# Kernel optimization log

Hardware: AMD Instinct MI355X
Metric: run time of the kernel (lower is better)

## Reference

```python
import jax, jax.numpy as jnp
import numpy as np

N = 100000
E = 1600000
IN_FEATS = 256
OUT_FEATS = 128
THRESHOLD = 0.5


def setup_inputs() -> dict:
    key = jax.random.key(0)
    k1, k2, k3, k4, k5, k6, k7 = jax.random.split(key, 7)
    return {
        "feat": jax.random.normal(k1, (N, IN_FEATS), dtype=jnp.float32),
        "src": jax.random.randint(k2, (E,), 0, N, dtype=jnp.int32),
        "dst": jax.random.randint(k3, (E,), 0, N, dtype=jnp.int32),
        "edge_weight": jax.random.uniform(k4, (E,), dtype=jnp.float32),
        "weight": jax.random.normal(k5, (IN_FEATS, OUT_FEATS), dtype=jnp.float32),
        "bias": jax.random.normal(k6, (OUT_FEATS,), dtype=jnp.float32),
        "mask_real": jax.random.uniform(k7, (IN_FEATS, OUT_FEATS), dtype=jnp.float32),
    }


def reference(feat, src, dst, edge_weight, weight, bias, mask_real):
    ones_e = jnp.ones((E,), dtype=feat.dtype)
    # norm == 'both': scale source feats by out_degree^-0.5 (clamped at 1)
    out_deg = jnp.clip(jax.ops.segment_sum(ones_e, src, num_segments=N), 1.0)
    feat_src = feat * (out_deg ** -0.5)[:, None]  # [N, IN]
    # binarized mask with straight-through estimator (training-mode path)
    hard = (mask_real > THRESHOLD).astype(mask_real.dtype)
    mask_t = jax.lax.stop_gradient(hard - mask_real) + mask_real
    w = mask_t * weight  # [IN, OUT]
    # in_feats > out_feats: project before aggregation
    feat_src = feat_src @ w  # [N, OUT]
    # u_mul_e then sum: gather source feats, scale by edge weight, scatter-add to dst
    msgs = feat_src[src] * edge_weight[:, None]  # [E, OUT]
    rst = jax.ops.segment_sum(msgs, dst, num_segments=N)  # [N, OUT]
    # norm == 'both': scale by in_degree^-0.5 (clamped at 1)
    in_deg = jnp.clip(jax.ops.segment_sum(ones_e, dst, num_segments=N), 1.0)
    rst = rst * (in_deg ** -0.5)[:, None]
    return rst + bias
```

## Files before the change

### kernel.cpp

```cpp
#include <hip/hip_runtime.h>

#define N_NODES 100000
#define N_EDGES 1600000
#define IN_F 256
#define OUT_F 128
#define NBUCK 391
#define NPART 256
#define CHUNK (N_EDGES / NPART)
#define BCAP 5632

#define ODW 25000
#define ODRB ((ODW + 255) / 256)

typedef __attribute__((ext_vector_type(8))) short short8;
typedef __attribute__((ext_vector_type(4))) float f32x4;

__device__ __forceinline__ unsigned bf16_rne(float f) {
    unsigned u = __float_as_uint(f);
    return (u + 0x7fffu + ((u >> 16) & 1u)) >> 16;
}

__global__ __launch_bounds__(256) void fused_pre_kernel(const int* __restrict__ src,
                                                        const int* __restrict__ dst,
                                                        const float* __restrict__ weight,
                                                        const float* __restrict__ mask_real,
                                                        unsigned* __restrict__ part,
                                                        unsigned* __restrict__ hist,
                                                        unsigned short* __restrict__ wmT) {
    __shared__ unsigned h[ODW];
    __shared__ unsigned hh[NBUCK];
    int b = blockIdx.x, t = threadIdx.x;
    for (int i = t; i < ODW; i += 256) h[i] = 0u;
    for (int i = t; i < NBUCK; i += 256) hh[i] = 0u;
    if (t < 128) {
        int i = b * 128 + t;
        int k = i >> 7, n = i & 127;
        float v = (mask_real[i] > 0.5f) ? weight[i] : 0.0f;
        wmT[(size_t)n * IN_F + k] = (unsigned short)bf16_rne(v);
    }
    __syncthreads();
    int base = b * CHUNK;
    for (int i = t; i < CHUNK; i += 256) {
        unsigned s = (unsigned)src[base + i];
        unsigned d = (unsigned)dst[base + i];
        atomicAdd(&h[s >> 2], 1u << ((s & 3u) * 8u));
        atomicAdd(&hh[d >> 8], 1u);
    }
    __syncthreads();
    unsigned* op = part + (size_t)b * ODW;
    for (int i = t; i < ODW; i += 256) op[i] = h[i];
    for (int i = t; i < NBUCK; i += 256) hist[(size_t)b * NBUCK + i] = hh[i];
}

__global__ __launch_bounds__(256) void fused_reduce_kernel(const unsigned* __restrict__ part,
                                                           const unsigned* __restrict__ hist,
                                                           unsigned* __restrict__ outpk,
                                                           unsigned* __restrict__ bsum) {
    int t = threadIdx.x;
    if (blockIdx.x < ODRB) {
        int d = blockIdx.x * 256 + t;
        if (d < ODW) {
            unsigned sum = 0u;
#pragma unroll 8
            for (int b = 0; b < NPART; b++) sum += part[(size_t)b * ODW + d];
            outpk[d] = sum;
        }
    } else {
        __shared__ unsigned red[256];
        int b = blockIdx.x - ODRB;
        red[t] = hist[(size_t)t * NBUCK + b];
        __syncthreads();
#pragma unroll
        for (int d = 128; d > 0; d >>= 1) {
            if (t < d) red[t] += red[t + d];
            __syncthreads();
        }
        if (t == 0) bsum[b] = red[0];
    }
}

__global__ __launch_bounds__(256) void scan_apply_kernel(const unsigned* __restrict__ hist,
                                                         const unsigned* __restrict__ bsum,
                                                         unsigned* __restrict__ scanned) {
    __shared__ unsigned red[256];
    __shared__ unsigned part[256];
    int b = blockIdx.x, t = threadIdx.x;
    unsigned loc = 0u;
    for (int i = t; i < b; i += 256) loc += bsum[i];
    red[t] = loc;
    __syncthreads();
#pragma unroll
    for (int d = 128; d > 0; d >>= 1) {
        if (t < d) red[t] += red[t + d];
        __syncthreads();
    }
    unsigned bpref = red[0];
    unsigned v = hist[(size_t)t * NBUCK + b];
    part[t] = v;
    __syncthreads();
#pragma unroll
    for (int d = 1; d < 256; d <<= 1) {
        unsigned x = (t >= d) ? part[t - d] : 0u;
        __syncthreads();
        part[t] += x;
        __syncthreads();
    }
    scanned[(size_t)b * 256 + t] = bpref + part[t] - v;
}

__global__ __launch_bounds__(256) void scatter_kernel(const int* __restrict__ src,
                                                      const int* __restrict__ dst,
                                                      const float* __restrict__ ew,
                                                      const unsigned* __restrict__ scanned,
                                                      uint2* __restrict__ tmp) {
    __shared__ unsigned cur[NBUCK];
    int p = blockIdx.x, t = threadIdx.x;
    for (int b = t; b < NBUCK; b += 256) cur[b] = scanned[(size_t)b * 256 + p];
    __syncthreads();
    int base = p * CHUNK;
    for (int i = t; i < CHUNK; i += 256) {
        int e = base + i;
        int s = src[e];
        int d = dst[e];
        unsigned pos = atomicAdd(&cur[(unsigned)d >> 8], 1u);
        tmp[pos] = make_uint2((unsigned)s | (((unsigned)d & 255u) << 17),
                              __float_as_uint(ew[e]));
    }
}

__global__ __launch_bounds__(256) void fillB_kernel(const uint2* __restrict__ tmp,
                                                    const unsigned* __restrict__ scanned,
                                                    unsigned* __restrict__ offsets,
                                                    unsigned* __restrict__ smeta) {
    __shared__ uint2 ebuf[BCAP];
    __shared__ unsigned hcnt[256];
    __shared__ unsigned pref[256];
    int b = blockIdx.x, t = threadIdx.x;
    unsigned base = scanned[(size_t)b * 256];
    unsigned next = (b == NBUCK - 1) ? (unsigned)N_EDGES : scanned[(size_t)(b + 1) * 256];
    int cnt = (int)(next - base);
    if (cnt > BCAP) cnt = BCAP;
    hcnt[t] = 0u;
    for (int i = t; i < cnt; i += 256) ebuf[i] = tmp[base + i];
    __syncthreads();
    for (int i = t; i < cnt; i += 256) atomicAdd(&hcnt[ebuf[i].x >> 17], 1u);
    __syncthreads();
    unsigned v = hcnt[t];
    pref[t] = v;
    __syncthreads();
#pragma unroll
    for (int d = 1; d < 256; d <<= 1) {
        unsigned x = (t >= d) ? pref[t - d] : 0u;
        __syncthreads();
        pref[t] += x;
        __syncthreads();
    }
    unsigned excl = pref[t] - v;
    int node = b * 256 + t;
    if (node <= N_NODES) offsets[node] = base + excl;
    hcnt[t] = base + excl;
    __syncthreads();
    for (int i = t; i < cnt; i += 256) {
        uint2 m = ebuf[i];
        unsigned pos = atomicAdd(&hcnt[m.x >> 17], 1u);
        smeta[pos] = ((m.y + 0x10000u) & 0xFFFE0000u) | (m.x & 0x1FFFFu);
    }
}

__global__ __launch_bounds__(256) void gemm_kernel(const float* __restrict__ feat,
                                                   const unsigned short* __restrict__ wmT,
                                                   const unsigned char* __restrict__ outdeg8,
                                                   unsigned short* __restrict__ hb) {
    __shared__ unsigned short sB[128][264];
    int t = threadIdx.x;
    for (int idx = t; idx < (128 * 256 / 8); idx += 256) {
        int flat = idx * 8;
        *(uint4*)&sB[flat >> 8][flat & 255] = *(const uint4*)&wmT[flat];
    }
    __syncthreads();

    int lane = t & 63, wv = t >> 6;
    int m16 = lane & 15, quad = lane >> 4;
    int row0 = blockIdx.x * 64;
    int arow = min(row0 + wv * 16 + m16, N_NODES - 1);
    const float* fp = feat + (size_t)arow * IN_F + quad * 8;

    float4 va[16];
#pragma unroll
    for (int i = 0; i < 8; i++) {
        va[2 * i]     = *(const float4*)(fp + i * 32);
        va[2 * i + 1] = *(const float4*)(fp + i * 32 + 4);
    }

    f32x4 acc[8];
#pragma unroll
    for (int i = 0; i < 8; i++) acc[i] = (f32x4){0.f, 0.f, 0.f, 0.f};

#pragma unroll
    for (int i = 0; i < 8; i++) {
        uint4 pk;
        pk.x = bf16_rne(va[2 * i].x) | (bf16_rne(va[2 * i].y) << 16);
        pk.y = bf16_rne(va[2 * i].z) | (bf16_rne(va[2 * i].w) << 16);
        pk.z = bf16_rne(va[2 * i + 1].x) | (bf16_rne(va[2 * i + 1].y) << 16);
        pk.w = bf16_rne(va[2 * i + 1].z) | (bf16_rne(va[2 * i + 1].w) << 16);
        short8 a;
        *(uint4*)&a = pk;
#pragma unroll
        for (int nt = 0; nt < 8; nt++) {
            short8 b = *(const short8*)&sB[nt * 16 + m16][i * 32 + quad * 8];
            acc[nt] = __builtin_amdgcn_mfma_f32_16x16x32_bf16(a, b, acc[nt], 0, 0, 0);
        }
    }
#pragma unroll
    for (int reg = 0; reg < 4; reg++) {
        int row = row0 + wv * 16 + quad * 4 + reg;
        if (row < N_NODES) {
            float s = rsqrtf(fmaxf((float)outdeg8[row], 1.0f));
#pragma unroll
            for (int nt = 0; nt < 8; nt++)
                hb[(size_t)row * OUT_F + nt * 16 + m16] =
                    (unsigned short)bf16_rne(acc[nt][reg] * s);
        }
    }
}

__global__ __launch_bounds__(256) void gather_kernel(const unsigned* __restrict__ smeta,
                                                     const unsigned* __restrict__ offsets,
                                                     const uint4* __restrict__ hrows4,
                                                     const float* __restrict__ bias,
                                                     float* __restrict__ out) {
    int lane = threadIdx.x & 63;
    int n = blockIdx.x * 4 + (threadIdx.x >> 6);
    int g = lane >> 4;
    int q = lane & 15;
    unsigned beg = offsets[n], end = offsets[n + 1];
    int deg = (int)(end - beg);

    float acc[8];
#pragma unroll
    for (int i = 0; i < 8; i++) acc[i] = 0.0f;

    for (int base = 0; base < deg; base += 64) {
        int c = min(64, deg - base);
        unsigned pv = 0u;
        if (lane < c) pv = smeta[beg + base + lane];
        int nch = (c + 3) >> 2;
#pragma unroll 4
        for (int j = 0; j < nch; j++) {
            int ei = (j << 2) + g;
            unsigned p = __shfl(pv, ei);
            unsigned s = p & 0x1FFFFu;
            float w = __uint_as_float(p & 0xFFFE0000u);
            uint4 h = hrows4[(size_t)s * 16u + q];
            acc[0] = fmaf(__uint_as_float(h.x << 16), w, acc[0]);
            acc[1] = fmaf(__uint_as_float(h.x & 0xffff0000u), w, acc[1]);
            acc[2] = fmaf(__uint_as_float(h.y << 16), w, acc[2]);
            acc[3] = fmaf(__uint_as_float(h.y & 0xffff0000u), w, acc[3]);
            acc[4] = fmaf(__uint_as_float(h.z << 16), w, acc[4]);
            acc[5] = fmaf(__uint_as_float(h.z & 0xffff0000u), w, acc[5]);
            acc[6] = fmaf(__uint_as_float(h.w << 16), w, acc[6]);
            acc[7] = fmaf(__uint_as_float(h.w & 0xffff0000u), w, acc[7]);
        }
    }

#pragma unroll
    for (int i = 0; i < 8; i++) {
        acc[i] += __shfl_xor(acc[i], 16);
        acc[i] += __shfl_xor(acc[i], 32);
    }

    float o0, o1;
    if (g == 0)      { o0 = acc[0]; o1 = acc[1]; }
    else if (g == 1) { o0 = acc[2]; o1 = acc[3]; }
    else if (g == 2) { o0 = acc[4]; o1 = acc[5]; }
    else             { o0 = acc[6]; o1 = acc[7]; }

    float sc = rsqrtf(fmaxf((float)deg, 1.0f));
    int col = q * 8 + g * 2;
    float2 b = *(const float2*)&bias[col];
    float2 o = make_float2(o0 * sc + b.x, o1 * sc + b.y);
    *(float2*)&out[(size_t)n * OUT_F + col] = o;
}

extern "C" void kernel_launch(void* const* d_in, const int* in_sizes, int n_in,
                              void* d_out, int out_size, void* d_ws, size_t ws_size,
                              hipStream_t stream) {
    const float* feat      = (const float*)d_in[0];
    const int*   src       = (const int*)d_in[1];
    const int*   dst       = (const int*)d_in[2];
    const float* ew        = (const float*)d_in[3];
    const float* weight    = (const float*)d_in[4];
    const float* bias      = (const float*)d_in[5];
    const float* mask_real = (const float*)d_in[6];
    float* out = (float*)d_out;

    char* ws = (char*)d_ws;
    size_t o = 0;
    auto take = [&](size_t bytes) {
        char* p = ws + o;
        o = (o + bytes + 255) & ~(size_t)255;
        return p;
    };
    unsigned short* wmT     = (unsigned short*)take((size_t)IN_F * OUT_F * 2);
    unsigned*       outpk   = (unsigned*)take((size_t)ODW * 4);
    unsigned*       offs    = (unsigned*)take((size_t)(N_NODES + 1) * 4);
    unsigned*       hist    = (unsigned*)take((size_t)NPART * NBUCK * 4);
    unsigned*       scanned = (unsigned*)take((size_t)NBUCK * 256 * 4);
    unsigned*       bsum    = (unsigned*)take((size_t)NBUCK * 4);
    uint2*          tmp     = (uint2*)take((size_t)N_EDGES * 8);
    unsigned*       smeta   = (unsigned*)take((size_t)N_EDGES * 4);
    unsigned short* hrows   = (unsigned short*)take((size_t)N_NODES * OUT_F * 2);

    unsigned* odpart = (unsigned*)tmp;

    fused_pre_kernel<<<NPART, 256, 0, stream>>>(src, dst, weight, mask_real,
                                                odpart, hist, wmT);
    fused_reduce_kernel<<<ODRB + NBUCK, 256, 0, stream>>>(odpart, hist, outpk, bsum);
    scan_apply_kernel<<<NBUCK, 256, 0, stream>>>(hist, bsum, scanned);
    scatter_kernel<<<NPART, 256, 0, stream>>>(src, dst, ew, scanned, tmp);
    gemm_kernel<<<(N_NODES + 63) / 64, 256, 0, stream>>>(feat, wmT,
                                                         (const unsigned char*)outpk, hrows);
    fillB_kernel<<<NBUCK, 256, 0, stream>>>(tmp, scanned, offs, smeta);
    gather_kernel<<<N_NODES / 4, 256, 0, stream>>>(smeta, offs,
                                                   (const uint4*)hrows, bias, out);
}
```

Measured before the change: 342.6 us.

## Fold scan pass into reduce and scatter, widen blocks to 512 threads

Removes the separate scan_apply kernel. Per-bucket column scans now happen in the reduce kernel, and each consumer rebuilds the bucket prefix itself: scatter does a 512-wide scan of bucket sums and fillB does a reduction. Thread counts in the pre, scatter and gemm kernels double to 512, and gemm now covers 128 rows per block. This saves one kernel launch and one dependent pass, at the price of scan work repeated in every scatter and fillB block.

```diff
diff --git a/kernel.cpp b/kernel.cpp
--- a/kernel.cpp
+++ b/kernel.cpp
@@ -20,7 +20,7 @@
     return (u + 0x7fffu + ((u >> 16) & 1u)) >> 16;
 }
 
-__global__ __launch_bounds__(256) void fused_pre_kernel(const int* __restrict__ src,
+__global__ __launch_bounds__(512) void fused_pre_kernel(const int* __restrict__ src,
                                                         const int* __restrict__ dst,
                                                         const float* __restrict__ weight,
                                                         const float* __restrict__ mask_real,
@@ -30,8 +30,8 @@
     __shared__ unsigned h[ODW];
     __shared__ unsigned hh[NBUCK];
     int b = blockIdx.x, t = threadIdx.x;
-    for (int i = t; i < ODW; i += 256) h[i] = 0u;
-    for (int i = t; i < NBUCK; i += 256) hh[i] = 0u;
+    for (int i = t; i < ODW; i += 512) h[i] = 0u;
+    for (int i = t; i < NBUCK; i += 512) hh[i] = 0u;
     if (t < 128) {
         int i = b * 128 + t;
         int k = i >> 7, n = i & 127;
@@ -40,7 +40,7 @@
     }
     __syncthreads();
     int base = b * CHUNK;
-    for (int i = t; i < CHUNK; i += 256) {
+    for (int i = t; i < CHUNK; i += 512) {
         unsigned s = (unsigned)src[base + i];
         unsigned d = (unsigned)dst[base + i];
         atomicAdd(&h[s >> 2], 1u << ((s & 3u) * 8u));
@@ -48,14 +48,16 @@
     }
     __syncthreads();
     unsigned* op = part + (size_t)b * ODW;
-    for (int i = t; i < ODW; i += 256) op[i] = h[i];
-    for (int i = t; i < NBUCK; i += 256) hist[(size_t)b * NBUCK + i] = hh[i];
+    for (int i = t; i < ODW; i += 512) op[i] = h[i];
+    for (int i = t; i < NBUCK; i += 512) hist[(size_t)b * NBUCK + i] = hh[i];
 }
 
 __global__ __launch_bounds__(256) void fused_reduce_kernel(const unsigned* __restrict__ part,
                                                            const unsigned* __restrict__ hist,
                                                            unsigned* __restrict__ outpk,
-                                                           unsigned* __restrict__ bsum) {
+                                                           unsigned* __restrict__ bsum,
+                                                           unsigned* __restrict__ colscan) {
+    __shared__ unsigned pscan[256];
     int t = threadIdx.x;
     if (blockIdx.x < ODRB) {
         int d = blockIdx.x * 256 + t;
@@ -66,59 +68,45 @@
             outpk[d] = sum;
         }
     } else {
-        __shared__ unsigned red[256];
         int b = blockIdx.x - ODRB;
-        red[t] = hist[(size_t)t * NBUCK + b];
-        __syncthreads();
-#pragma unroll
-        for (int d = 128; d > 0; d >>= 1) {
-            if (t < d) red[t] += red[t + d];
+        unsigned v = hist[(size_t)t * NBUCK + b];
+        pscan[t] = v;
+        __syncthreads();
+#pragma unroll
+        for (int d = 1; d < 256; d <<= 1) {
+            unsigned x = (t >= d) ? pscan[t - d] : 0u;
             __syncthreads();
-        }
-        if (t == 0) bsum[b] = red[0];
-    }
-}
-
-__global__ __launch_bounds__(256) void scan_apply_kernel(const unsigned* __restrict__ hist,
-                                                         const unsigned* __restrict__ bsum,
-                                                         unsigned* __restrict__ scanned) {
-    __shared__ unsigned red[256];
-    __shared__ unsigned part[256];
-    int b = blockIdx.x, t = threadIdx.x;
-    unsigned loc = 0u;
-    for (int i = t; i < b; i += 256) loc += bsum[i];
-    red[t] = loc;
-    __syncthreads();
-#pragma unroll
-    for (int d = 128; d > 0; d >>= 1) {
-        if (t < d) red[t] += red[t + d];
-        __syncthreads();
-    }
-    unsigned bpref = red[0];
-    unsigned v = hist[(size_t)t * NBUCK + b];
-    part[t] = v;
-    __syncthreads();
-#pragma unroll
-    for (int d = 1; d < 256; d <<= 1) {
-        unsigned x = (t >= d) ? part[t - d] : 0u;
-        __syncthreads();
-        part[t] += x;
-        __syncthreads();
-    }
-    scanned[(size_t)b * 256 + t] = bpref + part[t] - v;
-}
-
-__global__ __launch_bounds__(256) void scatter_kernel(const int* __restrict__ src,
+            pscan[t] += x;
+            __syncthreads();
+        }
+        colscan[(size_t)b * 256 + t] = pscan[t] - v;
+        if (t == 255) bsum[b] = pscan[255];
+    }
+}
+
+__global__ __launch_bounds__(512) void scatter_kernel(const int* __restrict__ src,
                                                       const int* __restrict__ dst,
                                                       const float* __restrict__ ew,
-                                                      const unsigned* __restrict__ scanned,
+                                                      const unsigned* __restrict__ colscan,
+                                                      const unsigned* __restrict__ bsum,
                                                       uint2* __restrict__ tmp) {
+    __shared__ unsigned sc[512];
     __shared__ unsigned cur[NBUCK];
     int p = blockIdx.x, t = threadIdx.x;
-    for (int b = t; b < NBUCK; b += 256) cur[b] = scanned[(size_t)b * 256 + p];
+    unsigned v = (t < NBUCK) ? bsum[t] : 0u;
+    sc[t] = v;
+    __syncthreads();
+#pragma unroll
+    for (int d = 1; d < 512; d <<= 1) {
+        unsigned x = (t >= d) ? sc[t - d] : 0u;
+        __syncthreads();
+        sc[t] += x;
+        __syncthreads();
+    }
+    if (t < NBUCK) cur[t] = (sc[t] - v) + colscan[(size_t)t * 256 + p];
     __syncthreads();
     int base = p * CHUNK;
-    for (int i = t; i < CHUNK; i += 256) {
+    for (int i = t; i < CHUNK; i += 512) {
         int e = base + i;
         int s = src[e];
         int d = dst[e];
@@ -129,15 +117,25 @@
 }
 
 __global__ __launch_bounds__(256) void fillB_kernel(const uint2* __restrict__ tmp,
-                                                    const unsigned* __restrict__ scanned,
+                                                    const unsigned* __restrict__ bsum,
                                                     unsigned* __restrict__ offsets,
                                                     unsigned* __restrict__ smeta) {
     __shared__ uint2 ebuf[BCAP];
     __shared__ unsigned hcnt[256];
     __shared__ unsigned pref[256];
+    __shared__ unsigned red[256];
     int b = blockIdx.x, t = threadIdx.x;
-    unsigned base = scanned[(size_t)b * 256];
-    unsigned next = (b == NBUCK - 1) ? (unsigned)N_EDGES : scanned[(size_t)(b + 1) * 256];
+    unsigned loc = 0u;
+    for (int i = t; i < b; i += 256) loc += bsum[i];
+    red[t] = loc;
+    __syncthreads();
+#pragma unroll
+    for (int d = 128; d > 0; d >>= 1) {
+        if (t < d) red[t] += red[t + d];
+        __syncthreads();
+    }
+    unsigned base = red[0];
+    unsigned next = base + bsum[b];
     int cnt = (int)(next - base);
     if (cnt > BCAP) cnt = BCAP;
     hcnt[t] = 0u;
@@ -167,13 +165,13 @@
     }
 }
 
-__global__ __launch_bounds__(256) void gemm_kernel(const float* __restrict__ feat,
+__global__ __launch_bounds__(512) void gemm_kernel(const float* __restrict__ feat,
                                                    const unsigned short* __restrict__ wmT,
                                                    const unsigned char* __restrict__ outdeg8,
                                                    unsigned short* __restrict__ hb) {
     __shared__ unsigned short sB[128][264];
     int t = threadIdx.x;
-    for (int idx = t; idx < (128 * 256 / 8); idx += 256) {
+    for (int idx = t; idx < (128 * 256 / 8); idx += 512) {
         int flat = idx * 8;
         *(uint4*)&sB[flat >> 8][flat & 255] = *(const uint4*)&wmT[flat];
     }
@@ -181,7 +179,7 @@
 
     int lane = t & 63, wv = t >> 6;
     int m16 = lane & 15, quad = lane >> 4;
-    int row0 = blockIdx.x * 64;
+    int row0 = blockIdx.x * 128;
     int arow = min(row0 + wv * 16 + m16, N_NODES - 1);
     const float* fp = feat + (size_t)arow * IN_F + quad * 8;
 
@@ -305,7 +303,7 @@
     unsigned*       outpk   = (unsigned*)take((size_t)ODW * 4);
     unsigned*       offs    = (unsigned*)take((size_t)(N_NODES + 1) * 4);
     unsigned*       hist    = (unsigned*)take((size_t)NPART * NBUCK * 4);
-    unsigned*       scanned = (unsigned*)take((size_t)NBUCK * 256 * 4);
+    unsigned*       colscan = (unsigned*)take((size_t)NBUCK * 256 * 4);
     unsigned*       bsum    = (unsigned*)take((size_t)NBUCK * 4);
     uint2*          tmp     = (uint2*)take((size_t)N_EDGES * 8);
     unsigned*       smeta   = (unsigned*)take((size_t)N_EDGES * 4);
@@ -313,14 +311,14 @@
 
     unsigned* odpart = (unsigned*)tmp;
 
-    fused_pre_kernel<<<NPART, 256, 0, stream>>>(src, dst, weight, mask_real,
+    fused_pre_kernel<<<NPART, 512, 0, stream>>>(src, dst, weight, mask_real,
                                                 odpart, hist, wmT);
-    fused_reduce_kernel<<<ODRB + NBUCK, 256, 0, stream>>>(odpart, hist, outpk, bsum);
-    scan_apply_kernel<<<NBUCK, 256, 0, stream>>>(hist, bsum, scanned);
-    scatter_kernel<<<NPART, 256, 0, stream>>>(src, dst, ew, scanned, tmp);
-    gemm_kernel<<<(N_NODES + 63) / 64, 256, 0, stream>>>(feat, wmT,
-                                                         (const unsigned char*)outpk, hrows);
-    fillB_kernel<<<NBUCK, 256, 0, stream>>>(tmp, scanned, offs, smeta);
+    fused_reduce_kernel<<<ODRB + NBUCK, 256, 0, stream>>>(odpart, hist, outpk,
+                                                          bsum, colscan);
+    scatter_kernel<<<NPART, 512, 0, stream>>>(src, dst, ew, colscan, bsum, tmp);
+    gemm_kernel<<<(N_NODES + 127) / 128, 512, 0, stream>>>(feat, wmT,
+                                                           (const unsigned char*)outpk, hrows);
+    fillB_kernel<<<NBUCK, 256, 0, stream>>>(tmp, bsum, offs, smeta);
     gather_kernel<<<N_NODES / 4, 256, 0, stream>>>(smeta, offs,
                                                    (const uint4*)hrows, bias, out);
 }
```

New measurement: 315.5 us. 7.9% less time.
